# Optimization experiments

Measured on AMD Instinct MI355X. Metric: run time of the kernel, lower is better.

Reference implementation:

```python
import jax, jax.numpy as jnp
import numpy as np

NUM_GRAPHS = 128
EPS = 1e-5  # torch BatchNorm1d default eps


def setup_inputs() -> dict:
    key = jax.random.key(0)
    ks = jax.random.split(key, 24)
    N, E, NHE = 50000, 800000, 50000
    NODE_RAW, HEDGE_RAW, H, HH, HOUT = 92, 40, 128, 128, 256
    s = 0.05
    inp = {
        "x": jax.random.normal(ks[0], (N, NODE_RAW), jnp.float32),
        "hedge_attrs": jax.random.normal(ks[1], (NHE, HEDGE_RAW), jnp.float32),
        "inter_relations_index": jax.random.randint(ks[2], (3, E), 0, N, jnp.int64),
        "batch": jax.random.randint(ks[3], (N,), 0, NUM_GRAPHS, jnp.int64),
        "num_nodes": N,
        # embed: Linear(92, h_dim)
        "embed_w": jax.random.normal(ks[4], (NODE_RAW, H), jnp.float32) * s,
        "embed_b": jax.random.normal(ks[5], (H,), jnp.float32) * s,
        # bembed: Linear(hedge_dim, hidden_hedge_dim)
        "bembed_w": jax.random.normal(ks[6], (HEDGE_RAW, HH), jnp.float32) * s,
        "bembed_b": jax.random.normal(ks[7], (HH,), jnp.float32) * s,
        # conv.lin_full_presplit: Linear(2H+HH, 2H)
        "lin_w": jax.random.normal(ks[8], (2 * H + HH, 2 * H), jnp.float32) * s,
        "lin_b": jax.random.normal(ks[9], (2 * H,), jnp.float32) * s,
        "bn1_g": jnp.ones((2 * H,), jnp.float32),
        "bn1_b": jnp.zeros((2 * H,), jnp.float32),
        "bn2_g": jnp.ones((H,), jnp.float32),
        "bn2_b": jnp.zeros((H,), jnp.float32),
        # learnable temperature of SoftmaxAggregation (init 1.0)
        "aggr_t": jnp.ones((), jnp.float32),
        "l1_w": jax.random.normal(ks[10], (H, HOUT), jnp.float32) * s,
        "l1_b": jax.random.normal(ks[11], (HOUT,), jnp.float32) * s,
        "out_w": jax.random.normal(ks[12], (HOUT, 1), jnp.float32) * s,
        "out_b": jax.random.normal(ks[13], (1,), jnp.float32) * s,
    }
    return inp


def _batchnorm(z, g, b):
    mu = z.mean(axis=0)
    var = z.var(axis=0)  # biased, matching torch training-mode normalization
    return (z - mu) * jax.lax.rsqrt(var + EPS) * g + b


def reference(x, hedge_attrs, inter_relations_index, batch, num_nodes,
              embed_w, embed_b, bembed_w, bembed_b, lin_w, lin_b,
              bn1_g, bn1_b, bn2_g, bn2_b, aggr_t, l1_w, l1_b, out_w, out_b):
    idx0 = inter_relations_index[0]
    idx1 = inter_relations_index[1]
    connect_feats = hedge_attrs @ bembed_w + bembed_b          # [NHE, HH]
    h = x @ embed_w + embed_b                                   # [N, H]

    # --- CHGInterConv ---
    origin = h[idx0]                                            # [E, H]
    connect = connect_feats[idx1]                               # [E, HH]
    remote = h[idx0]                                            # faithful to source (uses idx0)
    z = jnp.concatenate([origin, connect, remote], axis=1)      # [E, 2H+HH]
    z = z @ lin_w + lin_b                                       # [E, 2H]
    z = _batchnorm(z, bn1_g, bn1_b)
    z_f, z_c = jnp.split(z, 2, axis=-1)
    msg = jax.nn.sigmoid(z_f) * jax.nn.softplus(z_c)            # [E, H]

    # learned SoftmaxAggregation: per-node, per-channel segment softmax of t*msg
    alpha = msg * aggr_t
    m = jax.ops.segment_max(alpha, idx0, num_segments=num_nodes)
    m = jnp.where(jnp.isfinite(m), m, 0.0)                      # empty segments
    e = jnp.exp(alpha - m[idx0])
    denom = jax.ops.segment_sum(e, idx0, num_segments=num_nodes)
    w = e / (denom[idx0] + 1e-16)
    out = jax.ops.segment_sum(msg * w, idx0, num_segments=num_nodes)  # [N, H]

    out = _batchnorm(out, bn2_g, bn2_b)
    h = jax.nn.softplus(out + h)                                # residual + softplus

    # --- global mean pool over graphs ---
    counts = jax.ops.segment_sum(jnp.ones((num_nodes,), h.dtype), batch,
                                 num_segments=NUM_GRAPHS)
    pooled = jax.ops.segment_sum(h, batch, num_segments=NUM_GRAPHS)
    pooled = pooled / jnp.maximum(counts, 1.0)[:, None]         # [G, H]

    g = jax.nn.softplus(pooled @ l1_w + l1_b)                   # [G, HOUT]
    return g @ out_w + out_b                                    # [G, 1]
```

## Files before the change

kernel.cpp:

```cpp
#include <hip/hip_runtime.h>
#include <hip/hip_bf16.h>


#define EPS_BN 1e-5f
#define LOG2E 1.4426950408889634f
#define LN2   0.6931471805599453f

#define BIN_SH 8
#define BIN_CHUNK 4096

typedef __attribute__((ext_vector_type(8))) short bf16x8;
typedef __attribute__((ext_vector_type(4))) float f32x4;
typedef __attribute__((ext_vector_type(2))) float f32x2;

__device__ __forceinline__ float fexp2(float x) {
#if __has_builtin(__builtin_amdgcn_exp2f)
    return __builtin_amdgcn_exp2f(x);
#else
    return __expf(x * LN2);
#endif
}
__device__ __forceinline__ float flog2(float x) {
#if __has_builtin(__builtin_amdgcn_logf)
    return __builtin_amdgcn_logf(x);
#else
    return __logf(x) * LOG2E;
#endif
}
__device__ __forceinline__ float softplus_fast(float x) {
    return LN2 * flog2(1.f + fexp2(x * LOG2E));
}

__device__ __forceinline__ f32x2 pk_fma2(f32x2 a, f32x2 b, f32x2 c) {
#if __has_builtin(__builtin_elementwise_fma)
    return __builtin_elementwise_fma(a, b, c);
#else
    return (f32x2){fmaf(a.x, b.x, c.x), fmaf(a.y, b.y, c.y)};
#endif
}

__device__ __forceinline__ unsigned short f2bf(float f) {
    unsigned u = __float_as_uint(f);
    unsigned r = (u + 0x7fffu + ((u >> 16) & 1u)) >> 16;
    return (unsigned short)r;
}
__device__ __forceinline__ float bflo(unsigned u) { return __uint_as_float(u << 16); }
__device__ __forceinline__ float bfhi(unsigned u) { return __uint_as_float(u & 0xffff0000u); }
__device__ __forceinline__ float bfu16(unsigned short v) { return __uint_as_float(((unsigned)v) << 16); }
__device__ __forceinline__ unsigned pack2bf(float x, float y) {
    return (unsigned)f2bf(x) | ((unsigned)f2bf(y) << 16);
}

#if __has_builtin(__builtin_amdgcn_cvt_pk_f32_fp8) && __has_builtin(__builtin_amdgcn_cvt_pk_fp8_f32)
#define HW_FP8 1
#else
#define HW_FP8 0
#endif

__device__ __forceinline__ unsigned char f2fp8(float f) {
#if HW_FP8
    int r = __builtin_amdgcn_cvt_pk_fp8_f32(f, f, 0, false);
    return (unsigned char)(r & 0xff);
#else
    unsigned u = __float_as_uint(f);
    unsigned s = (u >> 24) & 0x80u;
    float af = fabsf(f);
    if (!(af >= 0.015625f)) {
        int m = (int)rintf(af * 512.f);
        if (m > 7) m = 7;
        return (unsigned char)(s | (unsigned)m);
    }
    if (af > 448.f) return (unsigned char)(s | 0x7e);
    unsigned au = __float_as_uint(af);
    unsigned r = au + 0x7ffffu + ((au >> 20) & 1u);
    int e8 = (int)(r >> 23) - 120;
    unsigned m = (r >> 20) & 7u;
    if (e8 > 15 || (e8 == 15 && m == 7)) return (unsigned char)(s | 0x7e);
    return (unsigned char)(s | ((unsigned)e8 << 3) | m);
#endif
}

__device__ __forceinline__ void fp8pair(unsigned p, f32x2& lo, f32x2& hi) {
#if HW_FP8
    lo = __builtin_amdgcn_cvt_pk_f32_fp8((int)p, false);
    hi = __builtin_amdgcn_cvt_pk_f32_fp8((int)p, true);
#else
    auto dec = [](unsigned byte) -> float {
        unsigned s = (byte & 0x80u) << 24;
        unsigned em = byte & 0x7fu;
        float nrm = __uint_as_float(s | ((em << 20) + 0x3C000000u));
        float sub = __uint_as_float(s | 0x3F800000u) * (float)em * 0.001953125f;
        return (em >= 8) ? nrm : sub;
    };
    lo = (f32x2){dec(p & 0xff), dec((p >> 8) & 0xff)};
    hi = (f32x2){dec((p >> 16) & 0xff), dec(p >> 24)};
#endif
}

__device__ __forceinline__ int perm256(int j) {
    return (j < 128) ? ((j >> 1) * 4 + (j & 1)) : (((j - 128) >> 1) * 4 + 2 + (j & 1));
}

__global__ __launch_bounds__(256) void k_prepw(const float* __restrict__ ew, const float* __restrict__ bw,
                                               const float* __restrict__ lw,
                                               unsigned short* __restrict__ embB, unsigned short* __restrict__ bembB,
                                               unsigned short* __restrict__ waB, unsigned short* __restrict__ wcB) {
    int i = blockIdx.x * 256 + threadIdx.x;
    if (i >= 81920) return;
    unsigned short* dst;
    int f, NKC, CT, mode;
    if (i < 12288)      { dst = embB;  f = i;         NKC = 3; CT = 2; mode = 0; }
    else if (i < 20480) { dst = bembB; f = i - 12288; NKC = 2; CT = 2; mode = 1; }
    else if (i < 53248) { dst = waB;   f = i - 20480; NKC = 4; CT = 4; mode = 2; }
    else                { dst = wcB;   f = i - 53248; NKC = 4; CT = 4; mode = 3; }
    int j = f & 7, l = (f >> 3) & 63;
    int r2 = f >> 9;
    int c = r2 % CT;
    int r3 = r2 / CT;
    int kc = r3 % NKC, w = r3 / NKC;
    int k = kc * 32 + ((l >> 4) & 3) * 8 + j;
    int n = (w * CT + c) * 16 + (l & 15);
    float v;
    if (mode == 0)      v = (k < 92) ? ew[k * 128 + n] : 0.f;
    else if (mode == 1) v = (k < 40) ? bw[k * 128 + n] : 0.f;
    else if (mode == 2) v = lw[k * 256 + n] + lw[(k + 256) * 256 + n];
    else                v = lw[(k + 128) * 256 + n];
    dst[f] = f2bf(v);
}

template<int KIN, int NKC1, int OMODE2>
__global__ __launch_bounds__(256) void mfma_fused(
    const float* __restrict__ in, const unsigned short* __restrict__ B1, const float* __restrict__ bias1,
    const unsigned short* __restrict__ B2, const float* __restrict__ bias2,
    unsigned short* __restrict__ hout, void* __restrict__ out2, int M,
    const int* __restrict__ aux_idx, int* __restrict__ aux_hist, int aux_cnt)
{
    const int r0 = blockIdx.x * 32;
    const int t = threadIdx.x;
    const int w = t >> 6;
    const int l = t & 63;
    const int m = l & 15, q = l >> 4;

    if (aux_idx) {
        const int T = gridDim.x * 256;
        for (int i = blockIdx.x * 256 + t; i < aux_cnt; i += T)
            atomicAdd(&aux_hist[aux_idx[i]], 1);
    }

    __shared__ __align__(16) unsigned short als[32 * NKC1 * 32];
    __shared__ __align__(16) unsigned short hls[32 * 136];

    const int KP = NKC1 * 32;
    for (int i = t; i < 32 * KP; i += 256) {
        int r = i / KP, k = i - r * KP;
        int gr = r0 + r;
        float v = (gr < M && k < KIN) ? in[(size_t)gr * KIN + k] : 0.f;
        int idx = (((r >> 4) * NKC1 + (k >> 5)) * 64 + ((k >> 3) & 3) * 16 + (r & 15)) * 8 + (k & 7);
        als[idx] = f2bf(v);
    }
    bf16x8 b1[NKC1][2];
    const bf16x8* B1f = (const bf16x8*)B1;
#pragma unroll
    for (int kc = 0; kc < NKC1; kc++)
#pragma unroll
        for (int c = 0; c < 2; c++)
            b1[kc][c] = B1f[((w * NKC1 + kc) * 2 + c) * 64 + l];
    __syncthreads();

    f32x4 acc1[2][2];
#pragma unroll
    for (int c = 0; c < 2; c++) { acc1[c][0] = (f32x4){0.f,0.f,0.f,0.f}; acc1[c][1] = (f32x4){0.f,0.f,0.f,0.f}; }
    const bf16x8* af = (const bf16x8*)als;
#pragma unroll
    for (int kc = 0; kc < NKC1; kc++) {
        bf16x8 a0 = af[kc * 64 + l];
        bf16x8 a1 = af[(NKC1 + kc) * 64 + l];
#pragma unroll
        for (int c = 0; c < 2; c++) {
            acc1[c][0] = __builtin_amdgcn_mfma_f32_16x16x32_bf16(a0, b1[kc][c], acc1[c][0], 0, 0, 0);
            acc1[c][1] = __builtin_amdgcn_mfma_f32_16x16x32_bf16(a1, b1[kc][c], acc1[c][1], 0, 0, 0);
        }
    }
#pragma unroll
    for (int c = 0; c < 2; c++) {
        int n1 = (w * 2 + c) * 16 + m;
        float bv = bias1[n1];
#pragma unroll
        for (int hh = 0; hh < 2; hh++) {
#pragma unroll
            for (int r = 0; r < 4; r++) {
                int row = hh * 16 + q * 4 + r;
                float val = acc1[c][hh][r] + bv;
                unsigned short bf = f2bf(val);
                hls[row * 136 + n1] = bf;
                if (OMODE2 == 1 && r0 + row < M) hout[(size_t)(r0 + row) * 128 + n1] = bf;
            }
        }
    }
    __syncthreads();

    bf16x8 b2[4][4];
    const bf16x8* B2f = (const bf16x8*)B2;
#pragma unroll
    for (int kc = 0; kc < 4; kc++)
#pragma unroll
        for (int c = 0; c < 4; c++)
            b2[kc][c] = B2f[((w * 4 + kc) * 4 + c) * 64 + l];

    f32x4 acc2[4][2];
#pragma unroll
    for (int c = 0; c < 4; c++) { acc2[c][0] = (f32x4){0.f,0.f,0.f,0.f}; acc2[c][1] = (f32x4){0.f,0.f,0.f,0.f}; }
#pragma unroll
    for (int kc = 0; kc < 4; kc++) {
        bf16x8 a0 = *(const bf16x8*)(hls + m * 136 + kc * 32 + q * 8);
        bf16x8 a1 = *(const bf16x8*)(hls + (m + 16) * 136 + kc * 32 + q * 8);
#pragma unroll
        for (int c = 0; c < 4; c++) {
            acc2[c][0] = __builtin_amdgcn_mfma_f32_16x16x32_bf16(a0, b2[kc][c], acc2[c][0], 0, 0, 0);
            acc2[c][1] = __builtin_amdgcn_mfma_f32_16x16x32_bf16(a1, b2[kc][c], acc2[c][1], 0, 0, 0);
        }
    }
#pragma unroll
    for (int c = 0; c < 4; c++) {
        int n = (w * 4 + c) * 16 + m;
        float bv = bias2 ? bias2[n] : 0.f;
        int pj = perm256(n);
#pragma unroll
        for (int hh = 0; hh < 2; hh++) {
#pragma unroll
            for (int r = 0; r < 4; r++) {
                int row = r0 + hh * 16 + q * 4 + r;
                if (row < M) {
                    float val = acc2[c][hh][r] + bv;
                    if (OMODE2 == 1) ((unsigned short*)out2)[(size_t)row * 256 + pj] = f2bf(val);
                    else             ((unsigned char*)out2)[(size_t)row * 256 + pj] = f2fp8(val);
                }
            }
        }
    }
}

__global__ __launch_bounds__(256) void k_scanA(const int* __restrict__ hist, int* __restrict__ rloc,
                                               int* __restrict__ bsum, int N) {
    __shared__ int s[256];
    const int t = threadIdx.x;
    const int n0 = blockIdx.x << 8;
    const int nn = min(N - n0, 256);
    int v = (t < nn) ? hist[n0 + t] : 0;
    s[t] = v;
    __syncthreads();
#pragma unroll
    for (int ofs = 1; ofs < 256; ofs <<= 1) {
        int u = (t >= ofs) ? s[t - ofs] : 0;
        __syncthreads();
        s[t] += u;
        __syncthreads();
    }
    if (t < nn) rloc[n0 + t] = s[t] - v;
    if (t == 255) bsum[blockIdx.x] = s[255];
}

__global__ __launch_bounds__(256) void k_scanB(const int* __restrict__ bsum, int* __restrict__ boff,
                                               const int* __restrict__ gcount, int* __restrict__ gptr, int NB) {
    __shared__ int s[256];
    const int t = threadIdx.x;
    int v = (t < NB) ? bsum[t] : 0;
    s[t] = v;
    __syncthreads();
#pragma unroll
    for (int ofs = 1; ofs < 256; ofs <<= 1) {
        int u = (t >= ofs) ? s[t - ofs] : 0;
        __syncthreads();
        s[t] += u;
        __syncthreads();
    }
    if (t < NB) boff[t] = s[t] - v;
    if (t == NB - 1) boff[NB] = s[t];
    __syncthreads();
    int gv = (t < 128) ? gcount[t] : 0;
    s[t] = gv;
    __syncthreads();
#pragma unroll
    for (int ofs = 1; ofs < 128; ofs <<= 1) {
        int u = (t >= ofs && t < 128) ? s[t - ofs] : 0;
        __syncthreads();
        if (t < 128) s[t] += u;
        __syncthreads();
    }
    if (t < 128) gptr[t + 1] = s[t];
    if (t == 0) gptr[0] = 0;
}

__global__ __launch_bounds__(256) void k_binA(
    const int* __restrict__ idx0, const int* __restrict__ idx1,
    const int* __restrict__ boff, const int* __restrict__ rloc,
    int* __restrict__ rowptr, int* __restrict__ bfill,
    int* __restrict__ staging,
    const int* __restrict__ batch, const int* __restrict__ gptr,
    int* __restrict__ gfill, int* __restrict__ gnodes,
    int E, int N, int NB, int EB, int GB)
{
    const int t = threadIdx.x;
    const int bid = blockIdx.x;
    if (bid >= EB + GB) {
        int i = ((bid - EB - GB) << 8) + t;
        if (i < N) rowptr[i] = boff[i >> BIN_SH] + rloc[i];
        if (bid == EB + GB && t == 0) rowptr[N] = boff[NB];
        return;
    }
    if (bid >= EB) {
        int i = (bid - EB) * 256 + t;
        if (i < N) {
            int g = batch[i];
            int pos = gptr[g] + atomicAdd(&gfill[g], 1);
            gnodes[pos] = i;
        }
        return;
    }
    __shared__ int svals[BIN_CHUNK];
    __shared__ unsigned char sbk[BIN_CHUNK];
    __shared__ int lhist[256], lbase[256];
    const int e0 = bid * BIN_CHUNK;
    const int cnt = min(E - e0, BIN_CHUNK);
    for (int b = t; b < NB; b += 256) lhist[b] = 0;
    __syncthreads();
    for (int i = t; i < cnt; i += 256) {
        int n = idx0[e0 + i];
        int m = idx1[e0 + i];
        int bk = n >> BIN_SH;
        sbk[i] = (unsigned char)bk;
        svals[i] = (m << BIN_SH) | (n & ((1 << BIN_SH) - 1));
        atomicAdd(&lhist[bk], 1);
    }
    __syncthreads();
    for (int b = t; b < NB; b += 256) {
        int h = lhist[b];
        int base = h ? atomicAdd(&bfill[b], h) : 0;
        lbase[b] = boff[b] + base;
        lhist[b] = 0;
    }
    __syncthreads();
    for (int i = t; i < cnt; i += 256) {
        int bk = sbk[i];
        int r = atomicAdd(&lhist[bk], 1);
        staging[lbase[bk] + r] = svals[i];
    }
}

__global__ __launch_bounds__(256) void k_build2(
    const int* __restrict__ rowptr, const int* __restrict__ staging,
    int* __restrict__ sidx1, int2* __restrict__ slots,
    const uint2* __restrict__ A16, const int* __restrict__ hist0,
    float* __restrict__ gsum, float* __restrict__ gsq,
    int E, int N, int per_slot, int nslots, int NB, int SL_BLOCKS)
{
    __shared__ float4 lsm4[256], lsq4[256];
    __shared__ int rp[257];
    __shared__ int lcnt[256];
    const int t = threadIdx.x;
    const int bid = blockIdx.x;

    if (bid < NB) {
        const int n0 = bid << BIN_SH;
        const int nn = min(N - n0, 256);
        for (int j = t; j <= nn; j += 256) rp[j] = rowptr[n0 + j];
        lcnt[t] = 0;
        __syncthreads();
        const int s0 = rp[0], s1 = rp[nn];
        for (int i = s0 + t; i < s1; i += 256) {
            int v = staging[i];
            int nl = v & 255;
            int r = atomicAdd(&lcnt[nl], 1);
            sidx1[rp[nl] + r] = v & 0xffffff00;
        }
        return;
    }
    if (bid < NB + SL_BLOCKS) {
        int s = (bid - NB) * 256 + t;
        if (s > nslots) return;
        long base = (long)s * per_slot;
        if (base >= E) { slots[s] = (int2){N, N - 1}; return; }
        int e0 = (int)base;
        int lo = 0, hi = N;
        while (lo + 1 < hi) { int mid = (lo + hi) >> 1; if (rowptr[mid] <= e0) lo = mid; else hi = mid; }
        int nS = lo;
        int nA = 0;
        if (e0 > 0) {
            lo = 0; hi = N;
            while (lo + 1 < hi) { int mid = (lo + hi) >> 1; if (rowptr[mid] < e0) lo = mid; else hi = mid; }
            nA = hi;
        }
        slots[s] = (int2){nA, nS};
        return;
    }
    const int s = t >> 6, l = t & 63;
    const int rb = bid - NB - SL_BLOCKS;
    const int w0 = rb * 4 + s;
    const int nw = (gridDim.x - NB - SL_BLOCKS) * 4;
    f32x2 smF = {0.f,0.f}, smC = {0.f,0.f}, sqF = {0.f,0.f}, sqC = {0.f,0.f};
    for (int n = w0; n < N; n += nw) {
        float dg = (float)hist0[n];
        uint2 a8 = A16[(size_t)n * 64 + l];
        f32x2 aF = {bflo(a8.x), bfhi(a8.x)};
        f32x2 aC = {bflo(a8.y), bfhi(a8.y)};
        f32x2 dF = aF * dg;
        f32x2 dC = aC * dg;
        smF += dF; smC += dC;
        sqF = pk_fma2(dF, aF, sqF);
        sqC = pk_fma2(dC, aC, sqC);
    }
    lsm4[t] = (float4){smF.x, smF.y, smC.x, smC.y};
    lsq4[t] = (float4){sqF.x, sqF.y, sqC.x, sqC.y};
    __syncthreads();
    const float* fm = (const float*)lsm4;
    const float* fq = (const float*)lsq4;
    float vs = fm[t] + fm[256 + t] + fm[512 + t] + fm[768 + t];
    float vq = fq[t] + fq[256 + t] + fq[512 + t] + fq[768 + t];
    atomicAdd(&gsum[t], vs);
    atomicAdd(&gsq[t], vq);
}

__global__ __launch_bounds__(256) void k_stats(const uint2* __restrict__ A16, const unsigned char* __restrict__ Cp8b,
                                               const int* __restrict__ rowptr, const int* __restrict__ sidx1,
                                               const int2* __restrict__ slots,
                                               float* __restrict__ gsum, float* __restrict__ gsq,
                                               int E, int N, int per_slot) {
    __shared__ float4 lsm4[256], lsq4[256];
    const int t = threadIdx.x;
    const int l = t & 63;
    const int wid = __builtin_amdgcn_readfirstlane(t >> 6);
    const int slot = blockIdx.x * 4 + wid;
    const unsigned lo4 = (unsigned)(l << 2);
    const long base = (long)slot * per_slot;
    const int e0 = (int)min((long)E, base);
    const int e1 = (int)min((long)E, base + per_slot);
    f32x2 smF = {0.f,0.f}, smC = {0.f,0.f};
    f32x2 sqF = {0.f,0.f}, sqC = {0.f,0.f};
    f32x2 csrF = {0.f,0.f}, csrC = {0.f,0.f};
    f32x2 aF2 = {0.f,0.f}, aC2 = {0.f,0.f};
    int cur_n = 0, bound = 0;

    auto flush = [&]() {
        smF += csrF; smC += csrC;
        sqF = pk_fma2(aF2, csrF, sqF);
        sqC = pk_fma2(aC2, csrC, sqC);
        csrF = (f32x2){0.f,0.f}; csrC = (f32x2){0.f,0.f};
    };
    auto loadA = [&](int n) {
        uint2 a8 = A16[(size_t)n * 64 + l];
        aF2 = (f32x2){bflo(a8.x) * 2.f, bfhi(a8.x) * 2.f};
        aC2 = (f32x2){bflo(a8.y) * 2.f, bfhi(a8.y) * 2.f};
    };

    if (e0 < e1) {
        cur_n = __builtin_amdgcn_readfirstlane(slots[slot].y);
        bound = __builtin_amdgcn_readfirstlane(rowptr[cur_n + 1]);
        loadA(cur_n);
    }

    auto proc = [&](int e, unsigned p) {
        if (e >= bound) {
            flush();
            do { cur_n++; bound = __builtin_amdgcn_readfirstlane(rowptr[cur_n + 1]); } while (bound <= e);
            loadA(cur_n);
        }
        f32x2 vf, vc;
        fp8pair(p, vf, vc);
        csrF += vf; csrC += vc;
        sqF = pk_fma2(vf, vf, sqF);
        sqC = pk_fma2(vc, vc, sqC);
    };

    int e = e0;
    for (; e + 8 <= e1; e += 8) {
        int4 mm0 = *(const int4*)(sidx1 + e);
        int4 mm1 = *(const int4*)(sidx1 + e + 4);
        unsigned p0 = *(const unsigned*)(Cp8b + ((unsigned)mm0.x + lo4));
        unsigned p1 = *(const unsigned*)(Cp8b + ((unsigned)mm0.y + lo4));
        unsigned p2 = *(const unsigned*)(Cp8b + ((unsigned)mm0.z + lo4));
        unsigned p3 = *(const unsigned*)(Cp8b + ((unsigned)mm0.w + lo4));
        unsigned p4 = *(const unsigned*)(Cp8b + ((unsigned)mm1.x + lo4));
        unsigned p5 = *(const unsigned*)(Cp8b + ((unsigned)mm1.y + lo4));
        unsigned p6 = *(const unsigned*)(Cp8b + ((unsigned)mm1.z + lo4));
        unsigned p7 = *(const unsigned*)(Cp8b + ((unsigned)mm1.w + lo4));
        proc(e, p0); proc(e + 1, p1); proc(e + 2, p2); proc(e + 3, p3);
        proc(e + 4, p4); proc(e + 5, p5); proc(e + 6, p6); proc(e + 7, p7);
    }
    for (; e < e1; e++) proc(e, *(const unsigned*)(Cp8b + ((unsigned)sidx1[e] + lo4)));
    flush();

    lsm4[t] = (float4){smF.x, smF.y, smC.x, smC.y};
    lsq4[t] = (float4){sqF.x, sqF.y, sqC.x, sqC.y};
    __syncthreads();
    const float* fm = (const float*)lsm4;
    const float* fq = (const float*)lsq4;
    float vs = fm[t] + fm[256 + t] + fm[512 + t] + fm[768 + t];
    float vq = fq[t] + fq[256 + t] + fq[512 + t] + fq[768 + t];
    atomicAdd(&gsum[t], vs);
    atomicAdd(&gsq[t], vq);
}

__global__ __launch_bounds__(256) void k_aggr(const uint2* __restrict__ A16, const unsigned char* __restrict__ Cp8b,
                                              const int* __restrict__ rowptr, const int* __restrict__ sidx1,
                                              const float* __restrict__ bn1_sum, const float* __restrict__ bn1_sq,
                                              const float* __restrict__ g1, const float* __restrict__ b1,
                                              const float* __restrict__ tptr, unsigned* __restrict__ out,
                                              float invE, int N) {
    const int t = threadIdx.x;
    const int l = t & 63;
    const int wid = __builtin_amdgcn_readfirstlane(t >> 6);
    const int n = blockIdx.x * 4 + wid;
    if (n >= N) return;

    const int e0 = __builtin_amdgcn_readfirstlane(rowptr[n]);
    const int e1 = __builtin_amdgcn_readfirstlane(rowptr[n + 1]);

    const float tt = tptr[0];
    const float4 sum4 = ((const float4*)bn1_sum)[l];
    const float4 sq4  = ((const float4*)bn1_sq)[l];
    const float2 gf = ((const float2*)g1)[l];
    const float2 gc = ((const float2*)(g1 + 128))[l];
    const float2 bf2 = ((const float2*)b1)[l];
    const float2 bc2 = ((const float2*)(b1 + 128))[l];
    auto mkss = [&](float sum, float sq, float gg, float bb, float& sc, float& sh) {
        float mu = sum * invE;
        float var = sq * invE - mu * mu;
        sc = gg * rsqrtf(var + EPS_BN);
        sh = fmaf(-mu, sc, bb);
    };
    float scx, shx, scy, shy, scz, shz, scw, shw;
    mkss(sum4.x, sq4.x, gf.x, bf2.x, scx, shx);
    mkss(sum4.y, sq4.y, gf.y, bf2.y, scy, shy);
    mkss(sum4.z, sq4.z, gc.x, bc2.x, scz, shz);
    mkss(sum4.w, sq4.w, gc.y, bc2.y, scw, shw);
    const f32x2 sF  = {-scx * LOG2E, -scy * LOG2E};
    const f32x2 sC  = { scz * LOG2E,  scw * LOG2E};

    uint2 a8 = A16[(size_t)n * 64 + l];
    f32x2 aF = {bflo(a8.x), bfhi(a8.x)}, aC = {bflo(a8.y), bfhi(a8.y)};
    const f32x2 bF = pk_fma2(aF, sF, (f32x2){-shx * LOG2E, -shy * LOG2E});
    const f32x2 bC = pk_fma2(aC, sC, (f32x2){ shz * LOG2E,  shw * LOG2E});

    if (e0 >= e1) { out[(size_t)n * 64 + l] = 0u; return; }

    const unsigned lo4 = (unsigned)(l << 2);
    f32x2 den = {0.f,0.f}, num = {0.f,0.f};

    auto G = [&](int e) -> unsigned {
        return *(const unsigned*)(Cp8b + ((unsigned)sidx1[e] + lo4));
    };
    auto procg = [&](unsigned p) {
        f32x2 vf, vc;
        fp8pair(p, vf, vc);
        f32x2 argf = pk_fma2(vf, sF, bF);
        f32x2 argc = pk_fma2(vc, sC, bC);
        f32x2 ef = {fexp2(argf.x), fexp2(argf.y)};
        f32x2 uu = {fexp2(argc.x), fexp2(argc.y)};
        f32x2 d1 = ef + 1.f;
        f32x2 u1 = uu + 1.f;
        f32x2 sig = {__builtin_amdgcn_rcpf(d1.x), __builtin_amdgcn_rcpf(d1.y)};
        f32x2 lg = {flog2(u1.x), flog2(u1.y)};
        f32x2 M = sig * lg;
        f32x2 tM = M * tt;
        f32x2 w = {fexp2(tM.x), fexp2(tM.y)};
        den += w;
        num = pk_fma2(M, w, num);
    };

    const int cnt = e1 - e0;
    unsigned cur[8];
#pragma unroll
    for (int i = 0; i < 8; i++)
        if (i < cnt) cur[i] = G(e0 + i);

    int e = e0;
    while (e + 8 < e1) {
        unsigned nxt[8];
#pragma unroll
        for (int i = 0; i < 8; i++)
            if (e + 8 + i < e1) nxt[i] = G(e + 8 + i);
#pragma unroll
        for (int i = 0; i < 8; i++) procg(cur[i]);
#pragma unroll
        for (int i = 0; i < 8; i++) cur[i] = nxt[i];
        e += 8;
    }
    const int rem = e1 - e;
#pragma unroll
    for (int i = 0; i < 8; i++)
        if (i < rem) procg(cur[i]);

    float ox = LN2 * num.x * __builtin_amdgcn_rcpf(den.x);
    float oy = LN2 * num.y * __builtin_amdgcn_rcpf(den.y);
    out[(size_t)n * 64 + l] = pack2bf(ox, oy);
}

__global__ __launch_bounds__(256) void k_bn2stats(const unsigned* __restrict__ outw, float* __restrict__ sum,
                                                  float* __restrict__ sq, int N) {
    __shared__ float4 ls[256];
    const int t = threadIdx.x;
    const int w = t & 63;
    const int rg = t >> 6;
    f32x2 sm = {0.f,0.f}, s2 = {0.f,0.f};
    for (int n = blockIdx.x * 4 + rg; n < N; n += gridDim.x * 4) {
        unsigned v = outw[(size_t)n * 64 + w];
        f32x2 x = {bflo(v), bfhi(v)};
        sm += x;
        s2 = pk_fma2(x, x, s2);
    }
    ls[t] = (float4){sm.x, sm.y, s2.x, s2.y};
    __syncthreads();
    if (t < 64) {
        float4 a = ls[t], b = ls[t + 64], c = ls[t + 128], d = ls[t + 192];
        atomicAdd(&sum[2 * w],     a.x + b.x + c.x + d.x);
        atomicAdd(&sum[2 * w + 1], a.y + b.y + c.y + d.y);
        atomicAdd(&sq[2 * w],      a.z + b.z + c.z + d.z);
        atomicAdd(&sq[2 * w + 1],  a.w + b.w + c.w + d.w);
    }
}

template<int SPLIT>
__global__ __launch_bounds__(128) void k_h2pool(const unsigned short* __restrict__ out,
                                                const unsigned short* __restrict__ h,
                                                const int* __restrict__ gptr, const int* __restrict__ gnodes,
                                                const float* __restrict__ bn2_sum, const float* __restrict__ bn2_sq,
                                                const float* __restrict__ g2, const float* __restrict__ b2,
                                                float* __restrict__ pooled, float invN) {
    const int g = blockIdx.x & 127;
    const int sp = blockIdx.x >> 7;
    const int c = threadIdx.x;
    float mu = bn2_sum[c] * invN;
    float var = bn2_sq[c] * invN - mu * mu;
    float sc = g2[c] * rsqrtf(var + EPS_BN);
    float sh = fmaf(-mu, sc, b2[c]);
    const int i0 = gptr[g], i1 = gptr[g + 1];
    float acc = 0.f;
    for (int i = i0 + sp; i < i1; i += SPLIT) {
        int n = gnodes[i];
        float v = fmaf(bfu16(out[(size_t)n * 128 + c]), sc, sh) + bfu16(h[(size_t)n * 128 + c]);
        acc += softplus_fast(v);
    }
    if (acc != 0.f) atomicAdd(&pooled[g * 128 + c], acc);
}

__global__ __launch_bounds__(256) void k_head(const float* __restrict__ pooled, const int* __restrict__ gcount,
                                              const float* __restrict__ l1w, const float* __restrict__ l1b,
                                              const float* __restrict__ outw, const float* __restrict__ outb,
                                              float* __restrict__ dout) {
    __shared__ float p[128];
    __shared__ float red[256];
    const int g = blockIdx.x;
    const int j = threadIdx.x;
    if (j < 128) {
        float cnt = (float)max(gcount[g], 1);
        p[j] = pooled[g * 128 + j] / cnt;
    }
    __syncthreads();
    float acc = l1b[j];
    for (int k = 0; k < 128; k++) acc = fmaf(p[k], l1w[k * 256 + j], acc);
    red[j] = softplus_fast(acc) * outw[j];
    __syncthreads();
    for (int s = 128; s > 0; s >>= 1) {
        if (j < s) red[j] += red[j + s];
        __syncthreads();
    }
    if (j == 0) dout[g] = red[0] + outb[0];
}

extern "C" void kernel_launch(void* const* d_in, const int* in_sizes, int n_in,
                              void* d_out, int out_size, void* d_ws, size_t ws_size,
                              hipStream_t stream) {
    const float* x        = (const float*)d_in[0];
    const float* hedge    = (const float*)d_in[1];
    const int*   iri      = (const int*)d_in[2];
    const int*   batch    = (const int*)d_in[3];
    const float* embed_w  = (const float*)d_in[5];
    const float* embed_b  = (const float*)d_in[6];
    const float* bembed_w = (const float*)d_in[7];
    const float* bembed_b = (const float*)d_in[8];
    const float* lin_w    = (const float*)d_in[9];
    const float* lin_b    = (const float*)d_in[10];
    const float* bn1_g    = (const float*)d_in[11];
    const float* bn1_b    = (const float*)d_in[12];
    const float* bn2_g    = (const float*)d_in[13];
    const float* bn2_b    = (const float*)d_in[14];
    const float* aggr_t   = (const float*)d_in[15];
    const float* l1_w     = (const float*)d_in[16];
    const float* l1_b     = (const float*)d_in[17];
    const float* out_w    = (const float*)d_in[18];
    const float* out_b    = (const float*)d_in[19];

    const int N   = in_sizes[0] / 92;
    const int NHE = in_sizes[1] / 40;
    const int E   = in_sizes[2] / 3;
    const int* idx0 = iri;
    const int* idx1 = iri + E;

    float* ws = (float*)d_ws;
    size_t off = 0;
    auto alloc = [&](size_t elems) -> float* {
        float* p = ws + off;
        off += (elems + 63) & ~(size_t)63;
        return p;
    };
    unsigned short* h16 = (unsigned short*)alloc((size_t)N * 64);
    uint2* A16    = (uint2*)alloc((size_t)N * 128);
    unsigned* Cp8 = (unsigned*)alloc((size_t)NHE * 64);
    unsigned short* embB  = (unsigned short*)alloc(6144);
    unsigned short* bembB = (unsigned short*)alloc(4096);
    unsigned short* waB   = (unsigned short*)alloc(16384);
    unsigned short* wcB   = (unsigned short*)alloc(16384);
    int*   rowptr = (int*)alloc((size_t)N + 1);
    int*   rloc   = (int*)alloc((size_t)N);
    int*   bsum   = (int*)alloc(256);
    int*   boff   = (int*)alloc(260);
    int*   sidx1  = (int*)alloc((size_t)E + 8);
    int*   staging = (int*)alloc((size_t)E + 8);
    int*   gptr   = (int*)alloc(129);
    int*   gnodes = (int*)alloc((size_t)N);
    unsigned* outbuf = (unsigned*)alloc((size_t)N * 64);
    int2*  slots  = (int2*)alloc(2 * 8200);
    float* zbase  = ws + off;
    int*   hist   = (int*)alloc((size_t)N);
    int*   bfill  = (int*)alloc(256);
    int*   gfill  = (int*)alloc(128);
    float* bn1_sum = alloc(256);
    float* bn1_sq  = alloc(256);
    float* bn2_sum = alloc(128);
    float* bn2_sq  = alloc(128);
    float* pooled  = alloc(128 * 128);
    int*   gcount  = (int*)alloc(128);
    size_t zbytes = (size_t)((ws + off) - zbase) * sizeof(float);
    (void)ws_size;

    hipMemsetAsync(zbase, 0, zbytes, stream);

    k_prepw<<<320, 256, 0, stream>>>(embed_w, bembed_w, lin_w, embB, bembB, waB, wcB);
    const int mtN   = (N + 31) / 32;
    const int mtNHE = (NHE + 31) / 32;
    mfma_fused<92, 3, 1><<<mtN, 256, 0, stream>>>(x, embB, embed_b, waB, lin_b, h16, A16, N,
                                                  idx0, hist, E);
    mfma_fused<40, 2, 2><<<mtNHE, 256, 0, stream>>>(hedge, bembB, bembed_b, wcB, nullptr, nullptr, Cp8, NHE,
                                                    batch, gcount, N);

    const int NB = (N + 255) >> BIN_SH;
    k_scanA<<<NB, 256, 0, stream>>>(hist, rloc, bsum, N);
    k_scanB<<<1, 256, 0, stream>>>(bsum, boff, gcount, gptr, NB);

    const int EB = (E + BIN_CHUNK - 1) / BIN_CHUNK;
    const int GB = (N + 255) / 256;
    k_binA<<<EB + GB + NB, 256, 0, stream>>>(idx0, idx1, boff, rloc, rowptr, bfill, staging,
                                             batch, gptr, gfill, gnodes, E, N, NB, EB, GB);

    const int EDGE_BLOCKS = 2048;
    const int NSLOTS = EDGE_BLOCKS * 4;
    int per_slot = ((E + NSLOTS - 1) / NSLOTS + 7) & ~7;
    int nslots_used = (E + per_slot - 1) / per_slot;

    const int SL_BLOCKS = (nslots_used + 1 + 255) / 256;
    const int RS_BLOCKS = 256;
    k_build2<<<NB + SL_BLOCKS + RS_BLOCKS, 256, 0, stream>>>(
        rowptr, staging, sidx1, slots, A16, hist, bn1_sum, bn1_sq,
        E, N, per_slot, nslots_used, NB, SL_BLOCKS);

    k_stats<<<EDGE_BLOCKS, 256, 0, stream>>>(A16, (const unsigned char*)Cp8, rowptr, sidx1, slots,
                                             bn1_sum, bn1_sq, E, N, per_slot);

    k_aggr<<<(N + 3) / 4, 256, 0, stream>>>(A16, (const unsigned char*)Cp8, rowptr, sidx1,
                                            bn1_sum, bn1_sq, bn1_g, bn1_b, aggr_t, outbuf,
                                            1.0f / (float)E, N);

    k_bn2stats<<<256, 256, 0, stream>>>((const unsigned*)outbuf, bn2_sum, bn2_sq, N);
    k_h2pool<16><<<128 * 16, 128, 0, stream>>>((const unsigned short*)outbuf, h16, gptr, gnodes,
                                               bn2_sum, bn2_sq, bn2_g, bn2_b, pooled, 1.0f / (float)N);

    k_head<<<128, 256, 0, stream>>>(pooled, gcount, l1_w, l1_b, out_w, out_b, (float*)d_out);
}
```

Measured before the change: 478.3 us.

## Compute BN1 stats directly from binned staging edges, drop separate stats kernel

Replaces the slot-based k_stats pass and the per-node degree-weighted term with a direct per-edge accumulation of (A+C) sum and square, read from the bucket-sorted staging array inside k_build2. This removes one kernel launch, the slot binary-search setup, and the dependency on the fully built sidx1. The stats now run concurrently with the sidx1 scatter blocks. In exchange, each edge gathers an A16 row as well as its fp8 C row, and bins of uneven size can leave the work unbalanced across blocks.

After: 495.7 us. 1.04x slower.

```diff
diff --git a/kernel.cpp b/kernel.cpp
--- a/kernel.cpp
+++ b/kernel.cpp
@@ -349,155 +349,81 @@
 
 __global__ __launch_bounds__(256) void k_build2(
     const int* __restrict__ rowptr, const int* __restrict__ staging,
-    int* __restrict__ sidx1, int2* __restrict__ slots,
-    const uint2* __restrict__ A16, const int* __restrict__ hist0,
+    const int* __restrict__ boff,
+    int* __restrict__ sidx1,
+    const uint2* __restrict__ A16, const unsigned char* __restrict__ Cp8b,
     float* __restrict__ gsum, float* __restrict__ gsq,
-    int E, int N, int per_slot, int nslots, int NB, int SL_BLOCKS)
+    int N, int NB, int NBp)
 {
-    __shared__ float4 lsm4[256], lsq4[256];
+    const int t = threadIdx.x;
+    const int bid = blockIdx.x;
+    const int ST = 4 * NBp;
+
+    if (bid < ST) {
+        __shared__ float4 lsm4[256], lsq4[256];
+        const int b = bid % NBp;
+        const int q = bid / NBp;
+        const int l = t & 63;
+        const int wid = __builtin_amdgcn_readfirstlane(t >> 6);
+        f32x2 smF = {0.f,0.f}, smC = {0.f,0.f}, sqF = {0.f,0.f}, sqC = {0.f,0.f};
+        if (b < NB) {
+            const int stream = q * 4 + wid;
+            const int s0 = __builtin_amdgcn_readfirstlane(boff[b]);
+            const int s1 = __builtin_amdgcn_readfirstlane(boff[b + 1]);
+            const unsigned lo4 = (unsigned)(l << 2);
+            const int abase = b << BIN_SH;
+
+            unsigned c0 = 0, c1 = 0, c2 = 0, c3 = 0;
+            uint2 a0 = {0,0}, a1 = {0,0}, a2 = {0,0}, a3 = {0,0};
+            int ip = s0 + stream;
+            int ld = ip;
+#define LDK(k) if (ld < s1) { int v = __builtin_amdgcn_readfirstlane(staging[ld]); \
+            c##k = *(const unsigned*)(Cp8b + (((unsigned)v & 0xffffff00u) + lo4)); \
+            a##k = A16[(size_t)(abase | (v & 255)) * 64 + l]; ld += 16; }
+#define PRK(k) { f32x2 vf, vc; fp8pair(c##k, vf, vc); \
+            f32x2 zF = (f32x2){bflo(a##k.x), bfhi(a##k.x)} + vf; \
+            f32x2 zC = (f32x2){bflo(a##k.y), bfhi(a##k.y)} + vc; \
+            smF += zF; smC += zC; \
+            sqF = pk_fma2(zF, zF, sqF); sqC = pk_fma2(zC, zC, sqC); }
+            LDK(0) LDK(1) LDK(2) LDK(3)
+            while (ip < s1) {
+                PRK(0); ip += 16; LDK(0)
+                if (ip >= s1) break;
+                PRK(1); ip += 16; LDK(1)
+                if (ip >= s1) break;
+                PRK(2); ip += 16; LDK(2)
+                if (ip >= s1) break;
+                PRK(3); ip += 16; LDK(3)
+            }
+#undef LDK
+#undef PRK
+        }
+        lsm4[t] = (float4){smF.x, smF.y, smC.x, smC.y};
+        lsq4[t] = (float4){sqF.x, sqF.y, sqC.x, sqC.y};
+        __syncthreads();
+        const float* fm = (const float*)lsm4;
+        const float* fq = (const float*)lsq4;
+        float vs = fm[t] + fm[256 + t] + fm[512 + t] + fm[768 + t];
+        float vq = fq[t] + fq[256 + t] + fq[512 + t] + fq[768 + t];
+        if (vs != 0.f) atomicAdd(&gsum[t], vs);
+        if (vq != 0.f) atomicAdd(&gsq[t], vq);
+        return;
+    }
     __shared__ int rp[257];
     __shared__ int lcnt[256];
-    const int t = threadIdx.x;
-    const int bid = blockIdx.x;
-
-    if (bid < NB) {
-        const int n0 = bid << BIN_SH;
-        const int nn = min(N - n0, 256);
-        for (int j = t; j <= nn; j += 256) rp[j] = rowptr[n0 + j];
-        lcnt[t] = 0;
-        __syncthreads();
-        const int s0 = rp[0], s1 = rp[nn];
-        for (int i = s0 + t; i < s1; i += 256) {
-            int v = staging[i];
-            int nl = v & 255;
-            int r = atomicAdd(&lcnt[nl], 1);
-            sidx1[rp[nl] + r] = v & 0xffffff00;
-        }
-        return;
-    }
-    if (bid < NB + SL_BLOCKS) {
-        int s = (bid - NB) * 256 + t;
-        if (s > nslots) return;
-        long base = (long)s * per_slot;
-        if (base >= E) { slots[s] = (int2){N, N - 1}; return; }
-        int e0 = (int)base;
-        int lo = 0, hi = N;
-        while (lo + 1 < hi) { int mid = (lo + hi) >> 1; if (rowptr[mid] <= e0) lo = mid; else hi = mid; }
-        int nS = lo;
-        int nA = 0;
-        if (e0 > 0) {
-            lo = 0; hi = N;
-            while (lo + 1 < hi) { int mid = (lo + hi) >> 1; if (rowptr[mid] < e0) lo = mid; else hi = mid; }
-            nA = hi;
-        }
-        slots[s] = (int2){nA, nS};
-        return;
-    }
-    const int s = t >> 6, l = t & 63;
-    const int rb = bid - NB - SL_BLOCKS;
-    const int w0 = rb * 4 + s;
-    const int nw = (gridDim.x - NB - SL_BLOCKS) * 4;
-    f32x2 smF = {0.f,0.f}, smC = {0.f,0.f}, sqF = {0.f,0.f}, sqC = {0.f,0.f};
-    for (int n = w0; n < N; n += nw) {
-        float dg = (float)hist0[n];
-        uint2 a8 = A16[(size_t)n * 64 + l];
-        f32x2 aF = {bflo(a8.x), bfhi(a8.x)};
-        f32x2 aC = {bflo(a8.y), bfhi(a8.y)};
-        f32x2 dF = aF * dg;
-        f32x2 dC = aC * dg;
-        smF += dF; smC += dC;
-        sqF = pk_fma2(dF, aF, sqF);
-        sqC = pk_fma2(dC, aC, sqC);
-    }
-    lsm4[t] = (float4){smF.x, smF.y, smC.x, smC.y};
-    lsq4[t] = (float4){sqF.x, sqF.y, sqC.x, sqC.y};
-    __syncthreads();
-    const float* fm = (const float*)lsm4;
-    const float* fq = (const float*)lsq4;
-    float vs = fm[t] + fm[256 + t] + fm[512 + t] + fm[768 + t];
-    float vq = fq[t] + fq[256 + t] + fq[512 + t] + fq[768 + t];
-    atomicAdd(&gsum[t], vs);
-    atomicAdd(&gsq[t], vq);
-}
-
-__global__ __launch_bounds__(256) void k_stats(const uint2* __restrict__ A16, const unsigned char* __restrict__ Cp8b,
-                                               const int* __restrict__ rowptr, const int* __restrict__ sidx1,
-                                               const int2* __restrict__ slots,
-                                               float* __restrict__ gsum, float* __restrict__ gsq,
-                                               int E, int N, int per_slot) {
-    __shared__ float4 lsm4[256], lsq4[256];
-    const int t = threadIdx.x;
-    const int l = t & 63;
-    const int wid = __builtin_amdgcn_readfirstlane(t >> 6);
-    const int slot = blockIdx.x * 4 + wid;
-    const unsigned lo4 = (unsigned)(l << 2);
-    const long base = (long)slot * per_slot;
-    const int e0 = (int)min((long)E, base);
-    const int e1 = (int)min((long)E, base + per_slot);
-    f32x2 smF = {0.f,0.f}, smC = {0.f,0.f};
-    f32x2 sqF = {0.f,0.f}, sqC = {0.f,0.f};
-    f32x2 csrF = {0.f,0.f}, csrC = {0.f,0.f};
-    f32x2 aF2 = {0.f,0.f}, aC2 = {0.f,0.f};
-    int cur_n = 0, bound = 0;
-
-    auto flush = [&]() {
-        smF += csrF; smC += csrC;
-        sqF = pk_fma2(aF2, csrF, sqF);
-        sqC = pk_fma2(aC2, csrC, sqC);
-        csrF = (f32x2){0.f,0.f}; csrC = (f32x2){0.f,0.f};
-    };
-    auto loadA = [&](int n) {
-        uint2 a8 = A16[(size_t)n * 64 + l];
-        aF2 = (f32x2){bflo(a8.x) * 2.f, bfhi(a8.x) * 2.f};
-        aC2 = (f32x2){bflo(a8.y) * 2.f, bfhi(a8.y) * 2.f};
-    };
-
-    if (e0 < e1) {
-        cur_n = __builtin_amdgcn_readfirstlane(slots[slot].y);
-        bound = __builtin_amdgcn_readfirstlane(rowptr[cur_n + 1]);
-        loadA(cur_n);
-    }
-
-    auto proc = [&](int e, unsigned p) {
-        if (e >= bound) {
-            flush();
-            do { cur_n++; bound = __builtin_amdgcn_readfirstlane(rowptr[cur_n + 1]); } while (bound <= e);
-            loadA(cur_n);
-        }
-        f32x2 vf, vc;
-        fp8pair(p, vf, vc);
-        csrF += vf; csrC += vc;
-        sqF = pk_fma2(vf, vf, sqF);
-        sqC = pk_fma2(vc, vc, sqC);
-    };
-
-    int e = e0;
-    for (; e + 8 <= e1; e += 8) {
-        int4 mm0 = *(const int4*)(sidx1 + e);
-        int4 mm1 = *(const int4*)(sidx1 + e + 4);
-        unsigned p0 = *(const unsigned*)(Cp8b + ((unsigned)mm0.x + lo4));
-        unsigned p1 = *(const unsigned*)(Cp8b + ((unsigned)mm0.y + lo4));
-        unsigned p2 = *(const unsigned*)(Cp8b + ((unsigned)mm0.z + lo4));
-        unsigned p3 = *(const unsigned*)(Cp8b + ((unsigned)mm0.w + lo4));
-        unsigned p4 = *(const unsigned*)(Cp8b + ((unsigned)mm1.x + lo4));
-        unsigned p5 = *(const unsigned*)(Cp8b + ((unsigned)mm1.y + lo4));
-        unsigned p6 = *(const unsigned*)(Cp8b + ((unsigned)mm1.z + lo4));
-        unsigned p7 = *(const unsigned*)(Cp8b + ((unsigned)mm1.w + lo4));
-        proc(e, p0); proc(e + 1, p1); proc(e + 2, p2); proc(e + 3, p3);
-        proc(e + 4, p4); proc(e + 5, p5); proc(e + 6, p6); proc(e + 7, p7);
-    }
-    for (; e < e1; e++) proc(e, *(const unsigned*)(Cp8b + ((unsigned)sidx1[e] + lo4)));
-    flush();
-
-    lsm4[t] = (float4){smF.x, smF.y, smC.x, smC.y};
-    lsq4[t] = (float4){sqF.x, sqF.y, sqC.x, sqC.y};
-    __syncthreads();
-    const float* fm = (const float*)lsm4;
-    const float* fq = (const float*)lsq4;
-    float vs = fm[t] + fm[256 + t] + fm[512 + t] + fm[768 + t];
-    float vq = fq[t] + fq[256 + t] + fq[512 + t] + fq[768 + t];
-    atomicAdd(&gsum[t], vs);
-    atomicAdd(&gsq[t], vq);
+    const int bb = bid - ST;
+    const int n0 = bb << BIN_SH;
+    const int nn = min(N - n0, 256);
+    for (int j = t; j <= nn; j += 256) rp[j] = rowptr[n0 + j];
+    lcnt[t] = 0;
+    __syncthreads();
+    const int s0 = rp[0], s1 = rp[nn];
+    for (int i = s0 + t; i < s1; i += 256) {
+        int v = staging[i];
+        int nl = v & 255;
+        int r = atomicAdd(&lcnt[nl], 1);
+        sidx1[rp[nl] + r] = v & 0xffffff00;
+    }
 }
 
 __global__ __launch_bounds__(256) void k_aggr(const uint2* __restrict__ A16, const unsigned char* __restrict__ Cp8b,
@@ -719,7 +645,6 @@
     int*   gptr   = (int*)alloc(129);
     int*   gnodes = (int*)alloc((size_t)N);
     unsigned* outbuf = (unsigned*)alloc((size_t)N * 64);
-    int2*  slots  = (int2*)alloc(2 * 8200);
     float* zbase  = ws + off;
     int*   hist   = (int*)alloc((size_t)N);
     int*   bfill  = (int*)alloc(256);
@@ -752,19 +677,10 @@
     k_binA<<<EB + GB + NB, 256, 0, stream>>>(idx0, idx1, boff, rloc, rowptr, bfill, staging,
                                              batch, gptr, gfill, gnodes, E, N, NB, EB, GB);
 
-    const int EDGE_BLOCKS = 2048;
-    const int NSLOTS = EDGE_BLOCKS * 4;
-    int per_slot = ((E + NSLOTS - 1) / NSLOTS + 7) & ~7;
-    int nslots_used = (E + per_slot - 1) / per_slot;
-
-    const int SL_BLOCKS = (nslots_used + 1 + 255) / 256;
-    const int RS_BLOCKS = 256;
-    k_build2<<<NB + SL_BLOCKS + RS_BLOCKS, 256, 0, stream>>>(
-        rowptr, staging, sidx1, slots, A16, hist, bn1_sum, bn1_sq,
-        E, N, per_slot, nslots_used, NB, SL_BLOCKS);
-
-    k_stats<<<EDGE_BLOCKS, 256, 0, stream>>>(A16, (const unsigned char*)Cp8, rowptr, sidx1, slots,
-                                             bn1_sum, bn1_sq, E, N, per_slot);
+    const int NBp = (NB + 7) & ~7;
+    k_build2<<<4 * NBp + NB, 256, 0, stream>>>(rowptr, staging, boff, sidx1,
+                                               A16, (const unsigned char*)Cp8,
+                                               bn1_sum, bn1_sq, N, NB, NBp);
 
     k_aggr<<<(N + 3) / 4, 256, 0, stream>>>(A16, (const unsigned char*)Cp8, rowptr, sidx1,
                                             bn1_sum, bn1_sq, bn1_g, bn1_b, aggr_t, outbuf,
```
